# Performance work log

Hardware: AMD Instinct MI355X
Metric: run time of the kernel (lower is better)

The kernel has to match this reference:

```python
import jax, jax.numpy as jnp
import numpy as np

DIM_INPUT = 1024
DIM_LATENT = 1024
DIM_HEAD = 64
INNER = max(DIM_INPUT, DIM_LATENT)  # 1024
HEADS = INNER // DIM_HEAD           # 16
SCALE = DIM_HEAD ** -0.5
RMS_EPS = 1e-8
LN_EPS = 1e-5


def layernorm(x, w, b):
    mu = jnp.mean(x, axis=-1, keepdims=True)
    var = jnp.var(x, axis=-1, keepdims=True)
    return (x - mu) * jax.lax.rsqrt(var + LN_EPS) * w + b


def rmsnorm(x, gamma):
    # x / clamp(||x||_2 * d^-0.5, eps) * gamma  (per-head, last dim = DIM_HEAD)
    norm = jnp.linalg.norm(x, axis=-1, keepdims=True) * (DIM_HEAD ** -0.5)
    return x / jnp.maximum(norm, RMS_EPS) * gamma


def setup_inputs() -> dict:
    key = jax.random.key(0)
    ks = jax.random.split(key, 10)
    b, n, m = 4, 2048, 256
    x = jax.random.normal(ks[0], (b, n, DIM_INPUT), dtype=jnp.float32)
    latents_c1 = jax.random.normal(ks[1], (b, m, DIM_LATENT), dtype=jnp.float32)
    latents_c0 = jax.random.normal(ks[2], (b, m, DIM_LATENT), dtype=jnp.float32)
    consciousness_mask = jax.random.randint(ks[3], (b, n), 0, 2).astype(bool)
    s = 0.02
    Wq = jax.random.normal(ks[4], (DIM_LATENT, INNER), dtype=jnp.float32) * s
    Wkv = jax.random.normal(ks[5], (DIM_INPUT, 2 * INNER), dtype=jnp.float32) * s
    Wout = jax.random.normal(ks[6], (INNER, DIM_LATENT), dtype=jnp.float32) * s
    bout = jnp.zeros((DIM_LATENT,), dtype=jnp.float32)
    ln_x_w = jnp.ones((DIM_INPUT,), dtype=jnp.float32)
    ln_x_b = jnp.zeros((DIM_INPUT,), dtype=jnp.float32)
    ln_l_w = jnp.ones((DIM_LATENT,), dtype=jnp.float32)
    ln_l_b = jnp.zeros((DIM_LATENT,), dtype=jnp.float32)
    gamma_q = jnp.ones((DIM_HEAD,), dtype=jnp.float32)
    gamma_k = jnp.ones((DIM_HEAD,), dtype=jnp.float32)
    return dict(x=x, latents_c1=latents_c1, latents_c0=latents_c0,
                consciousness_mask=consciousness_mask,
                ln_x_w=ln_x_w, ln_x_b=ln_x_b, ln_l_w=ln_l_w, ln_l_b=ln_l_b,
                gamma_q=gamma_q, gamma_k=gamma_k,
                Wq=Wq, Wkv=Wkv, Wout=Wout, bout=bout)


def reference(x, latents_c1, latents_c0, consciousness_mask,
              ln_x_w, ln_x_b, ln_l_w, ln_l_b, gamma_q, gamma_k,
              Wq, Wkv, Wout, bout):
    b, n, _ = x.shape
    m = latents_c1.shape[1]
    x = layernorm(x, ln_x_w, ln_x_b)
    l1 = layernorm(latents_c1, ln_l_w, ln_l_b)
    l0 = layernorm(latents_c0, ln_l_w, ln_l_b)

    # projections -> heads
    q1 = (l1 @ Wq).reshape(b, m, HEADS, DIM_HEAD).transpose(0, 2, 1, 3)  # b h m d
    q0 = (l0 @ Wq).reshape(b, m, HEADS, DIM_HEAD).transpose(0, 2, 1, 3)
    kv = x @ Wkv                                                         # b n 2*inner
    k, v = jnp.split(kv, 2, axis=-1)
    k = k.reshape(b, n, HEADS, DIM_HEAD).transpose(0, 2, 1, 3)           # b h n d
    v = v.reshape(b, n, HEADS, DIM_HEAD).transpose(0, 2, 1, 3)

    qn1 = rmsnorm(q1, gamma_q) * SCALE
    qn0 = rmsnorm(q0, gamma_q) * SCALE
    kn = rmsnorm(k, gamma_k)

    attn1 = jnp.einsum('bhid,bhjd->bhij', qn1, kn)
    attn0 = jnp.einsum('bhid,bhjd->bhij', qn0, kn)

    neg = -jnp.finfo(attn1.dtype).max
    attn1 = jnp.where(consciousness_mask[:, None, None, :], attn1, neg)
    # NOTE: source only masks the c1 stream; c0 is left unmasked (faithful).

    attn1 = jax.nn.softmax(attn1, axis=-1)
    attn0 = jax.nn.softmax(attn0, axis=-1)

    o1 = jnp.einsum('bhij,bhjd->bhid', attn1, v).transpose(0, 2, 1, 3).reshape(b, m, INNER)
    o0 = jnp.einsum('bhij,bhjd->bhid', attn0, v).transpose(0, 2, 1, 3).reshape(b, m, INNER)
    return (o1 @ Wout + bout, o0 @ Wout + bout)
```

## Files before the change

kernel.cpp:

```cpp
#include <hip/hip_runtime.h>
#include <hip/hip_bf16.h>
#include <float.h>
#include <math.h>

#define BB 4
#define NN 2048
#define MM 256
#define DIN 1024
#define INNER 1024
#define NHEADS 16
#define DHEAD 64

typedef __attribute__((ext_vector_type(8))) short bf16x8;
typedef __attribute__((ext_vector_type(4))) float f32x4;
typedef __attribute__((ext_vector_type(4))) unsigned int u32x4;

__device__ __forceinline__ unsigned short f2bf(float f) {
    unsigned int u = __builtin_bit_cast(unsigned int, f);
    u = (u + 0x7fffu + ((u >> 16) & 1u)) >> 16;
    return (unsigned short)u;
}

__device__ __forceinline__ float fexp2(float x) {
#if __has_builtin(__builtin_amdgcn_exp2f)
    return __builtin_amdgcn_exp2f(x);
#else
    float r; asm("v_exp_f32 %0, %1" : "=v"(r) : "v"(x)); return r;
#endif
}

__device__ __forceinline__ unsigned int cvt_pk_bf16(float a, float b) {
    unsigned int r;
    asm("v_cvt_pk_bf16_f32 %0, %1, %2" : "=v"(r) : "v"(a), "v"(b));
    return r;
}

__device__ __forceinline__ void gload_lds16(const void* g, void* l) {
    __builtin_amdgcn_global_load_lds((__attribute__((address_space(1))) void*)(g),
                                     (__attribute__((address_space(3))) void*)(l),
                                     16, 0, 0);
}

#define LOG2E 1.4426950408889634f

__device__ __forceinline__ void ln_row(const float* __restrict__ srow,
                                       unsigned short* __restrict__ drow,
                                       const float* __restrict__ w,
                                       const float* __restrict__ bv) {
    const int tid = threadIdx.x;
    const float4 v = ((const float4*)srow)[tid];
    float sum = v.x + v.y + v.z + v.w;
    float sq  = v.x * v.x + v.y * v.y + v.z * v.z + v.w * v.w;
    #pragma unroll
    for (int off = 32; off; off >>= 1) {
        sum += __shfl_down(sum, off);
        sq  += __shfl_down(sq, off);
    }
    __shared__ float ls[4], lq[4];
    const int wv = tid >> 6;
    if ((tid & 63) == 0) { ls[wv] = sum; lq[wv] = sq; }
    __syncthreads();
    sum = ls[0] + ls[1] + ls[2] + ls[3];
    sq  = lq[0] + lq[1] + lq[2] + lq[3];
    const float mu  = sum * (1.0f / 1024.0f);
    const float var = sq * (1.0f / 1024.0f) - mu * mu;
    const float rs  = rsqrtf(var + 1e-5f);
    const float4 w4 = ((const float4*)w)[tid];
    const float4 b4 = ((const float4*)bv)[tid];
    ushort4 o;
    o.x = f2bf((v.x - mu) * rs * w4.x + b4.x);
    o.y = f2bf((v.y - mu) * rs * w4.y + b4.y);
    o.z = f2bf((v.z - mu) * rs * w4.z + b4.z);
    o.w = f2bf((v.w - mu) * rs * w4.w + b4.w);
    ((ushort4*)drow)[tid] = o;
}

__global__ __launch_bounds__(256) void ln_bf16_kernel(const float* __restrict__ src,
                                                      unsigned short* __restrict__ dst,
                                                      const float* __restrict__ w,
                                                      const float* __restrict__ bv) {
    const int row = blockIdx.x;
    ln_row(src + (size_t)row * 1024, dst + (size_t)row * 1024, w, bv);
}

__global__ __launch_bounds__(256) void ln2_bf16_kernel(const float* __restrict__ src1,
                                                       const float* __restrict__ src2,
                                                       int split,
                                                       unsigned short* __restrict__ dst,
                                                       const float* __restrict__ w,
                                                       const float* __restrict__ bv) {
    const int row = blockIdx.x;
    const float* s = (row < split) ? (src1 + (size_t)row * 1024)
                                   : (src2 + (size_t)(row - split) * 1024);
    ln_row(s, dst + (size_t)row * 1024, w, bv);
}

__global__ __launch_bounds__(256) void transpose_cast_kernel(const float* __restrict__ W,
                                                             unsigned short* __restrict__ WT,
                                                             int K, int N) {
    __shared__ float t[32][33];
    const int k0 = blockIdx.y * 32, n0 = blockIdx.x * 32;
    const int tx = threadIdx.x & 31, ty8 = threadIdx.x >> 5;
    #pragma unroll
    for (int i = 0; i < 4; i++) {
        const int k = ty8 + i * 8;
        t[k][tx] = W[(size_t)(k0 + k) * N + n0 + tx];
    }
    __syncthreads();
    #pragma unroll
    for (int i = 0; i < 4; i++) {
        const int n = ty8 + i * 8;
        WT[(size_t)(n0 + n) * K + k0 + tx] = f2bf(t[tx][n]);
    }
}

__global__ __launch_bounds__(256) void v_transpose_bf16(const unsigned short* __restrict__ vbh,
                                                        unsigned short* __restrict__ vth) {
    __shared__ unsigned short t[32][34];
    const int n0 = blockIdx.x * 32;
    const int d0 = blockIdx.y * 32;
    const int bh = blockIdx.z;
    const int b = bh >> 4, h = bh & 15;
    const int tx = threadIdx.x & 31, ty8 = threadIdx.x >> 5;
    #pragma unroll
    for (int i = 0; i < 4; i++) {
        const int nr = ty8 + i * 8;
        t[nr][tx] = vbh[(size_t)(b * NN + n0 + nr) * 1024 + h * 64 + d0 + tx];
    }
    __syncthreads();
    #pragma unroll
    for (int i = 0; i < 4; i++) {
        const int dr = ty8 + i * 8;
        vth[((size_t)(b * 16 + h) * 64 + d0 + dr) * 2048 + n0 + tx] = t[tx][dr];
    }
}

#define GEMM_STAGE(AS, BS, kt)                                                        \
    {                                                                                 \
        _Pragma("unroll")                                                             \
        for (int e = 0; e < 2; e++) {                                                 \
            const int r0 = (w * 2 + e) * 16;                                          \
            gload_lds16(Ag + (size_t)(r0 + srow) * K + (kt) + selt, &AS[r0 * 32]);    \
            gload_lds16(Bg + (size_t)(r0 + srow) * K + (kt) + selt, &BS[r0 * 32]);    \
        }                                                                             \
    }

#define GEMM_COMPUTE(AS, BS)                                                          \
    {                                                                                 \
        bf16x8 af[4], bfv[4];                                                         \
        _Pragma("unroll")                                                             \
        for (int m = 0; m < 4; m++)                                                   \
            af[m] = *(const bf16x8*)&AS[(wr * 64 + m * 16 + (l & 15)) * 32 + (l >> 4) * 8]; \
        _Pragma("unroll")                                                             \
        for (int n = 0; n < 4; n++)                                                   \
            bfv[n] = *(const bf16x8*)&BS[(wc * 64 + n * 16 + (l & 15)) * 32 + (l >> 4) * 8]; \
        _Pragma("unroll")                                                             \
        for (int m = 0; m < 4; m++)                                                   \
            _Pragma("unroll")                                                         \
            for (int n = 0; n < 4; n++)                                               \
                acc[m][n] = __builtin_amdgcn_mfma_f32_16x16x32_bf16(af[m], bfv[n], acc[m][n], 0, 0, 0); \
    }

template<int MODE>
__global__ __launch_bounds__(256) void gemm_bf16_kernel(const unsigned short* __restrict__ A,
                                                        const unsigned short* __restrict__ BT,
                                                        float* __restrict__ C,
                                                        unsigned short* __restrict__ outK,
                                                        unsigned short* __restrict__ outV,
                                                        int M, int N, int K,
                                                        const float* __restrict__ aux) {
    __shared__ __align__(16) unsigned short As0[128 * 32];
    __shared__ __align__(16) unsigned short As1[128 * 32];
    __shared__ __align__(16) unsigned short Bs0[128 * 32];
    __shared__ __align__(16) unsigned short Bs1[128 * 32];
    const int tid = threadIdx.x;
    const int l = tid & 63, w = tid >> 6;
    const int wr = w >> 1, wc = w & 1;

    const int gx = gridDim.x;
    const int flat = blockIdx.y * gx + blockIdx.x;
    const int cpx = (gx * gridDim.y) >> 3;
    const int swz = (flat & 7) * cpx + (flat >> 3);
    const int rb = (swz / gx) * 128, cb = (swz % gx) * 128;

    f32x4 acc[4][4];
    #pragma unroll
    for (int m = 0; m < 4; m++)
        #pragma unroll
        for (int n = 0; n < 4; n++) acc[m][n] = (f32x4){0.0f, 0.0f, 0.0f, 0.0f};

    const int srow = l >> 2;
    const int selt = (l & 3) * 8;
    const unsigned short* Ag = A + (size_t)rb * K;
    const unsigned short* Bg = BT + (size_t)cb * K;

    GEMM_STAGE(As0, Bs0, 0);
    __syncthreads();
    int kt = 0;
    for (; kt + 64 < K; kt += 64) {
        GEMM_STAGE(As1, Bs1, kt + 32);
        GEMM_COMPUTE(As0, Bs0);
        __syncthreads();
        GEMM_STAGE(As0, Bs0, kt + 64);
        GEMM_COMPUTE(As1, Bs1);
        __syncthreads();
    }
    GEMM_STAGE(As1, Bs1, kt + 32);
    GEMM_COMPUTE(As0, Bs0);
    __syncthreads();
    GEMM_COMPUTE(As1, Bs1);

    const int lx = l & 15;
    const int col0 = cb + wc * 64;
    const int row0 = rb + wr * 64 + (l >> 4) * 4;

    if constexpr (MODE == 0) {
        #pragma unroll
        for (int m = 0; m < 4; m++) {
            #pragma unroll
            for (int n = 0; n < 4; n++) {
                const int col = col0 + n * 16 + lx;
                const float badd = aux[col];
                #pragma unroll
                for (int r = 0; r < 4; r++)
                    C[(size_t)(row0 + m * 16 + r) * N + col] = acc[m][n][r] + badd;
            }
        }
    } else {
        const bool isK = (MODE == 2) || (col0 < (N >> 1));
        if (isK) {
            float g4[4];
            #pragma unroll
            for (int n = 0; n < 4; n++) g4[n] = aux[n * 16 + lx];
            const float fin = (MODE == 2) ? (0.125f * LOG2E) : 1.0f;
            #pragma unroll
            for (int m = 0; m < 4; m++) {
                #pragma unroll
                for (int r = 0; r < 4; r++) {
                    float ss = 0.0f;
                    #pragma unroll
                    for (int n = 0; n < 4; n++) ss += acc[m][n][r] * acc[m][n][r];
                    ss += __shfl_xor(ss, 1);
                    ss += __shfl_xor(ss, 2);
                    ss += __shfl_xor(ss, 4);
                    ss += __shfl_xor(ss, 8);
                    const float inv = fin / fmaxf(sqrtf(ss) * 0.125f, 1e-8f);
                    const size_t rbase = (size_t)(row0 + m * 16 + r) * 1024 + col0;
                    #pragma unroll
                    for (int n = 0; n < 4; n++)
                        outK[rbase + n * 16 + lx] = f2bf(acc[m][n][r] * inv * g4[n]);
                }
            }
        } else {
            const int colv = col0 - 1024;
            #pragma unroll
            for (int m = 0; m < 4; m++) {
                #pragma unroll
                for (int r = 0; r < 4; r++) {
                    const size_t rbase = (size_t)(row0 + m * 16 + r) * 1024 + colv;
                    #pragma unroll
                    for (int n = 0; n < 4; n++)
                        outV[rbase + n * 16 + lx] = f2bf(acc[m][n][r]);
                }
            }
        }
    }
}

__global__ __launch_bounds__(256) void attn_mfma_kernel(const unsigned short* __restrict__ qbh,
                                                        const unsigned short* __restrict__ kbh,
                                                        const unsigned short* __restrict__ vth,
                                                        const int* __restrict__ mask,
                                                        unsigned short* __restrict__ obuf) {
    const int bh = blockIdx.x;
    const int qt = blockIdx.y;
    const int sid = blockIdx.z;
    const int b = bh >> 4, h = bh & 15;
    const int tid = threadIdx.x;
    const int l = tid & 63, w = tid >> 6;
    const int lq = l & 15, g = l >> 4;

    __shared__ unsigned short Ks[64 * 64];
    __shared__ unsigned short Vts[64 * 64];
    __shared__ int Ms[64];

    bf16x8 aq[2];
    const size_t qrow = (size_t)((sid * BB + b) * MM + qt * 64 + w * 16 + lq);
    #pragma unroll
    for (int ks = 0; ks < 2; ks++)
        aq[ks] = *(const bf16x8*)&qbh[qrow * 1024 + h * 64 + ks * 32 + g * 8];

    f32x4 oacc[4];
    #pragma unroll
    for (int n = 0; n < 4; n++) oacc[n] = (f32x4){0.0f, 0.0f, 0.0f, 0.0f};
    float mrun = -FLT_MAX, lrun = 0.0f;

    for (int t0 = 0; t0 < NN; t0 += 64) {
        #pragma unroll
        for (int e = 0; e < 2; e++) {
            const int L = tid + 256 * e;
            const int row = L >> 3, c8 = L & 7;
            const bf16x8 kv8 = *(const bf16x8*)&kbh[(size_t)(b * NN + t0 + row) * 1024 + h * 64 + c8 * 8];
            *(bf16x8*)&Ks[row * 64 + ((c8 ^ (row & 7)) * 8)] = kv8;
            const bf16x8 vv8 = *(const bf16x8*)&vth[((size_t)(b * 16 + h) * 64 + row) * 2048 + t0 + c8 * 8];
            *(bf16x8*)&Vts[row * 64 + ((c8 ^ (row & 7)) * 8)] = vv8;
        }
        if (tid < 64) Ms[tid] = mask[b * NN + t0 + tid];
        __syncthreads();

        f32x4 st[4];
        #pragma unroll
        for (int j = 0; j < 4; j++) st[j] = (f32x4){0.0f, 0.0f, 0.0f, 0.0f};
        #pragma unroll
        for (int j = 0; j < 4; j++) {
            #pragma unroll
            for (int ks = 0; ks < 2; ks++) {
                const int row = j * 16 + lq;
                const bf16x8 kf = *(const bf16x8*)&Ks[row * 64 + (((ks * 4 + g) ^ (row & 7)) * 8)];
                st[j] = __builtin_amdgcn_mfma_f32_16x16x32_bf16(kf, aq[ks], st[j], 0, 0, 0);
            }
        }

        float p[4][4];
        if (sid == 0) {
            #pragma unroll
            for (int j = 0; j < 4; j++)
                #pragma unroll
                for (int r = 0; r < 4; r++)
                    p[j][r] = (Ms[j * 16 + g * 4 + r] == 0) ? -3.0e38f : st[j][r];
        } else {
            #pragma unroll
            for (int j = 0; j < 4; j++)
                #pragma unroll
                for (int r = 0; r < 4; r++) p[j][r] = st[j][r];
        }

        float mloc = fmaxf(fmaxf(p[0][0], p[0][1]), fmaxf(p[0][2], p[0][3]));
        #pragma unroll
        for (int j = 1; j < 4; j++)
            mloc = fmaxf(mloc, fmaxf(fmaxf(p[j][0], p[j][1]), fmaxf(p[j][2], p[j][3])));
        mloc = fmaxf(mloc, __shfl_xor(mloc, 16));
        mloc = fmaxf(mloc, __shfl_xor(mloc, 32));

        if (__any(mloc > mrun + 8.0f)) {
            const float mn = fmaxf(mrun, mloc);
            const float scal = fexp2(mrun - mn);
            mrun = mn;
            lrun *= scal;
            float oscal[4];
            #pragma unroll
            for (int r = 0; r < 4; r++) oscal[r] = __shfl(scal, g * 4 + r);
            #pragma unroll
            for (int n = 0; n < 4; n++)
                #pragma unroll
                for (int r = 0; r < 4; r++) oacc[n][r] *= oscal[r];
        }

        float rsum = 0.0f;
        #pragma unroll
        for (int j = 0; j < 4; j++)
            #pragma unroll
            for (int r = 0; r < 4; r++) { p[j][r] = fexp2(p[j][r] - mrun); rsum += p[j][r]; }
        rsum += __shfl_xor(rsum, 16);
        rsum += __shfl_xor(rsum, 32);
        lrun += rsum;

        unsigned int packed[4][2];
        #pragma unroll
        for (int jt = 0; jt < 4; jt++)
            #pragma unroll
            for (int hh = 0; hh < 2; hh++)
                packed[jt][hh] = cvt_pk_bf16(p[jt][2 * hh], p[jt][2 * hh + 1]);

        #pragma unroll
        for (int ks = 0; ks < 2; ks++) {
            unsigned int wds[4];
            #pragma unroll
            for (int wd = 0; wd < 4; wd++) {
                const int src = lq + 16 * ((g & 1) * 2 + (wd >> 1));
                const unsigned int vA = (unsigned int)__shfl((int)packed[ks * 2][wd & 1], src);
                const unsigned int vB = (unsigned int)__shfl((int)packed[ks * 2 + 1][wd & 1], src);
                wds[wd] = (g & 2) ? vB : vA;
            }
            const u32x4 tmp = {wds[0], wds[1], wds[2], wds[3]};
            const bf16x8 afP = __builtin_bit_cast(bf16x8, tmp);
            #pragma unroll
            for (int n = 0; n < 4; n++) {
                const int drow = n * 16 + lq;
                const bf16x8 bv = *(const bf16x8*)&Vts[drow * 64 + (((ks * 4 + g) ^ (drow & 7)) * 8)];
                oacc[n] = __builtin_amdgcn_mfma_f32_16x16x32_bf16(afP, bv, oacc[n], 0, 0, 0);
            }
        }
        __syncthreads();
    }

    const float il = 1.0f / lrun;
    float linv[4];
    #pragma unroll
    for (int r = 0; r < 4; r++) linv[r] = __shfl(il, g * 4 + r);
    unsigned short* ob = obuf + ((size_t)((sid * BB + b) * MM + qt * 64 + w * 16)) * 1024 + h * 64;
    #pragma unroll
    for (int n = 0; n < 4; n++)
        #pragma unroll
        for (int r = 0; r < 4; r++)
            ob[(size_t)(g * 4 + r) * 1024 + n * 16 + lq] = f2bf(oacc[n][r] * linv[r]);
}

extern "C" void kernel_launch(void* const* d_in, const int* in_sizes, int n_in,
                              void* d_out, int out_size, void* d_ws, size_t ws_size,
                              hipStream_t stream) {
    const float* x      = (const float*)d_in[0];
    const float* lc1    = (const float*)d_in[1];
    const float* lc0    = (const float*)d_in[2];
    const int*   mask   = (const int*)d_in[3];
    const float* ln_x_w = (const float*)d_in[4];
    const float* ln_x_b = (const float*)d_in[5];
    const float* ln_l_w = (const float*)d_in[6];
    const float* ln_l_b = (const float*)d_in[7];
    const float* g_q    = (const float*)d_in[8];
    const float* g_k    = (const float*)d_in[9];
    const float* Wq     = (const float*)d_in[10];
    const float* Wkv    = (const float*)d_in[11];
    const float* Wout   = (const float*)d_in[12];
    const float* bout   = (const float*)d_in[13];
    float* out = (float*)d_out;

    char* p = (char*)d_ws;
    unsigned short* xnb   = (unsigned short*)p; p += (size_t)8388608 * 2;
    unsigned short* latb  = (unsigned short*)p; p += (size_t)2097152 * 2;
    unsigned short* obb   = (unsigned short*)p; p += (size_t)2097152 * 2;
    unsigned short* WkvT  = (unsigned short*)p; p += (size_t)2097152 * 2;
    unsigned short* WqT   = (unsigned short*)p; p += (size_t)1048576 * 2;
    unsigned short* WoutT = (unsigned short*)p; p += (size_t)1048576 * 2;
    unsigned short* qbh   = (unsigned short*)p; p += (size_t)2097152 * 2;
    unsigned short* kbh   = (unsigned short*)p; p += (size_t)8388608 * 2;
    unsigned short* vbh   = (unsigned short*)p; p += (size_t)8388608 * 2;
    unsigned short* vth   = (unsigned short*)p; p += (size_t)8388608 * 2;

    ln_bf16_kernel<<<BB * NN, 256, 0, stream>>>(x, xnb, ln_x_w, ln_x_b);
    ln2_bf16_kernel<<<2 * BB * MM, 256, 0, stream>>>(lc1, lc0, BB * MM, latb, ln_l_w, ln_l_b);

    transpose_cast_kernel<<<dim3(2048 / 32, 1024 / 32), 256, 0, stream>>>(Wkv, WkvT, 1024, 2048);
    transpose_cast_kernel<<<dim3(1024 / 32, 1024 / 32), 256, 0, stream>>>(Wq, WqT, 1024, 1024);
    transpose_cast_kernel<<<dim3(1024 / 32, 1024 / 32), 256, 0, stream>>>(Wout, WoutT, 1024, 1024);

    gemm_bf16_kernel<1><<<dim3(2048 / 128, 8192 / 128), 256, 0, stream>>>(
        xnb, WkvT, nullptr, kbh, vbh, 8192, 2048, 1024, g_k);
    gemm_bf16_kernel<2><<<dim3(1024 / 128, 2048 / 128), 256, 0, stream>>>(
        latb, WqT, nullptr, qbh, nullptr, 2048, 1024, 1024, g_q);

    v_transpose_bf16<<<dim3(NN / 32, 2, BB * NHEADS), 256, 0, stream>>>(vbh, vth);

    attn_mfma_kernel<<<dim3(BB * NHEADS, MM / 64, 2), 256, 0, stream>>>(qbh, kbh, vth, mask, obb);

    gemm_bf16_kernel<0><<<dim3(1024 / 128, 2048 / 128), 256, 0, stream>>>(
        obb, WoutT, out, nullptr, nullptr, 2048, 1024, 1024, bout);
}
```

Before: 280.6 us.

## Double-buffer K/V tiles in attention and use smaller GEMM row tiles

The attention kernel now prefetches the next K, V and mask tile into registers while computing on the current LDS buffer. It writes them to a second LDS buffer, so each iteration needs one barrier instead of two. The Q-projection and output GEMMs become templated on BM and use 64-row tiles, doubling block count for these small (2048-row) GEMMs to fill more CUs. The trade-offs are more LDS and register use in attention and lower per-block reuse in the smaller GEMM tiles.

```diff
diff --git a/kernel.cpp b/kernel.cpp
--- a/kernel.cpp
+++ b/kernel.cpp
@@ -138,30 +138,34 @@
 #define GEMM_STAGE(AS, BS, kt)                                                        \
     {                                                                                 \
         _Pragma("unroll")                                                             \
+        for (int e = 0; e < EA; e++) {                                                \
+            const int r0 = (w * EA + e) * 16;                                         \
+            gload_lds16(Ag + (size_t)(r0 + srow) * K + (kt) + selt, &AS[r0 * 32]);    \
+        }                                                                             \
+        _Pragma("unroll")                                                             \
         for (int e = 0; e < 2; e++) {                                                 \
             const int r0 = (w * 2 + e) * 16;                                          \
-            gload_lds16(Ag + (size_t)(r0 + srow) * K + (kt) + selt, &AS[r0 * 32]);    \
             gload_lds16(Bg + (size_t)(r0 + srow) * K + (kt) + selt, &BS[r0 * 32]);    \
         }                                                                             \
     }
 
 #define GEMM_COMPUTE(AS, BS)                                                          \
     {                                                                                 \
-        bf16x8 af[4], bfv[4];                                                         \
+        bf16x8 af[MREP], bfv[4];                                                      \
         _Pragma("unroll")                                                             \
-        for (int m = 0; m < 4; m++)                                                   \
-            af[m] = *(const bf16x8*)&AS[(wr * 64 + m * 16 + (l & 15)) * 32 + (l >> 4) * 8]; \
+        for (int m = 0; m < MREP; m++)                                                \
+            af[m] = *(const bf16x8*)&AS[(wr * (BM / 2) + m * 16 + (l & 15)) * 32 + (l >> 4) * 8]; \
         _Pragma("unroll")                                                             \
         for (int n = 0; n < 4; n++)                                                   \
             bfv[n] = *(const bf16x8*)&BS[(wc * 64 + n * 16 + (l & 15)) * 32 + (l >> 4) * 8]; \
         _Pragma("unroll")                                                             \
-        for (int m = 0; m < 4; m++)                                                   \
+        for (int m = 0; m < MREP; m++)                                                \
             _Pragma("unroll")                                                         \
             for (int n = 0; n < 4; n++)                                               \
                 acc[m][n] = __builtin_amdgcn_mfma_f32_16x16x32_bf16(af[m], bfv[n], acc[m][n], 0, 0, 0); \
     }
 
-template<int MODE>
+template<int MODE, int BM>
 __global__ __launch_bounds__(256) void gemm_bf16_kernel(const unsigned short* __restrict__ A,
                                                         const unsigned short* __restrict__ BT,
                                                         float* __restrict__ C,
@@ -169,8 +173,10 @@
                                                         unsigned short* __restrict__ outV,
                                                         int M, int N, int K,
                                                         const float* __restrict__ aux) {
-    __shared__ __align__(16) unsigned short As0[128 * 32];
-    __shared__ __align__(16) unsigned short As1[128 * 32];
+    constexpr int MREP = BM / 32;
+    constexpr int EA = BM / 64;
+    __shared__ __align__(16) unsigned short As0[BM * 32];
+    __shared__ __align__(16) unsigned short As1[BM * 32];
     __shared__ __align__(16) unsigned short Bs0[128 * 32];
     __shared__ __align__(16) unsigned short Bs1[128 * 32];
     const int tid = threadIdx.x;
@@ -181,11 +187,11 @@
     const int flat = blockIdx.y * gx + blockIdx.x;
     const int cpx = (gx * gridDim.y) >> 3;
     const int swz = (flat & 7) * cpx + (flat >> 3);
-    const int rb = (swz / gx) * 128, cb = (swz % gx) * 128;
-
-    f32x4 acc[4][4];
-    #pragma unroll
-    for (int m = 0; m < 4; m++)
+    const int rb = (swz / gx) * BM, cb = (swz % gx) * 128;
+
+    f32x4 acc[MREP][4];
+    #pragma unroll
+    for (int m = 0; m < MREP; m++)
         #pragma unroll
         for (int n = 0; n < 4; n++) acc[m][n] = (f32x4){0.0f, 0.0f, 0.0f, 0.0f};
 
@@ -212,11 +218,11 @@
 
     const int lx = l & 15;
     const int col0 = cb + wc * 64;
-    const int row0 = rb + wr * 64 + (l >> 4) * 4;
+    const int row0 = rb + wr * (BM / 2) + (l >> 4) * 4;
 
     if constexpr (MODE == 0) {
         #pragma unroll
-        for (int m = 0; m < 4; m++) {
+        for (int m = 0; m < MREP; m++) {
             #pragma unroll
             for (int n = 0; n < 4; n++) {
                 const int col = col0 + n * 16 + lx;
@@ -234,7 +240,7 @@
             for (int n = 0; n < 4; n++) g4[n] = aux[n * 16 + lx];
             const float fin = (MODE == 2) ? (0.125f * LOG2E) : 1.0f;
             #pragma unroll
-            for (int m = 0; m < 4; m++) {
+            for (int m = 0; m < MREP; m++) {
                 #pragma unroll
                 for (int r = 0; r < 4; r++) {
                     float ss = 0.0f;
@@ -254,7 +260,7 @@
         } else {
             const int colv = col0 - 1024;
             #pragma unroll
-            for (int m = 0; m < 4; m++) {
+            for (int m = 0; m < MREP; m++) {
                 #pragma unroll
                 for (int r = 0; r < 4; r++) {
                     const size_t rbase = (size_t)(row0 + m * 16 + r) * 1024 + colv;
@@ -280,9 +286,8 @@
     const int l = tid & 63, w = tid >> 6;
     const int lq = l & 15, g = l >> 4;
 
-    __shared__ unsigned short Ks[64 * 64];
-    __shared__ unsigned short Vts[64 * 64];
-    __shared__ int Ms[64];
+    __shared__ __align__(16) unsigned short KVs[2][8192];
+    __shared__ int Ms[2][64];
 
     bf16x8 aq[2];
     const size_t qrow = (size_t)((sid * BB + b) * MM + qt * 64 + w * 16 + lq);
@@ -290,23 +295,48 @@
     for (int ks = 0; ks < 2; ks++)
         aq[ks] = *(const bf16x8*)&qbh[qrow * 1024 + h * 64 + ks * 32 + g * 8];
 
+    const int srow0 = tid >> 3, srow1 = (tid >> 3) + 32, sc8 = tid & 7;
+    const unsigned short* kgb = kbh + (size_t)(b * NN) * 1024 + h * 64;
+    const unsigned short* vgb = vth + ((size_t)(b * 16 + h) * 64) * 2048;
+    bf16x8 kreg0, kreg1, vreg0, vreg1;
+    int mreg = 0;
+
+#define ATT_LOAD(t0)                                                                  \
+    {                                                                                 \
+        kreg0 = *(const bf16x8*)&kgb[(size_t)((t0) + srow0) * 1024 + sc8 * 8];        \
+        kreg1 = *(const bf16x8*)&kgb[(size_t)((t0) + srow1) * 1024 + sc8 * 8];        \
+        vreg0 = *(const bf16x8*)&vgb[(size_t)srow0 * 2048 + (t0) + sc8 * 8];          \
+        vreg1 = *(const bf16x8*)&vgb[(size_t)srow1 * 2048 + (t0) + sc8 * 8];          \
+        if (tid < 64) mreg = mask[b * NN + (t0) + tid];                               \
+    }
+
+#define ATT_WRITE(buf)                                                                \
+    {                                                                                 \
+        unsigned short* kd = &KVs[buf][0];                                            \
+        *(bf16x8*)&kd[srow0 * 64 + ((sc8 ^ (srow0 & 7)) * 8)] = kreg0;                \
+        *(bf16x8*)&kd[srow1 * 64 + ((sc8 ^ (srow1 & 7)) * 8)] = kreg1;                \
+        unsigned short* vd = &KVs[buf][4096];                                         \
+        *(bf16x8*)&vd[srow0 * 64 + ((sc8 ^ (srow0 & 7)) * 8)] = vreg0;                \
+        *(bf16x8*)&vd[srow1 * 64 + ((sc8 ^ (srow1 & 7)) * 8)] = vreg1;                \
+        if (tid < 64) Ms[buf][tid] = mreg;                                            \
+    }
+
     f32x4 oacc[4];
     #pragma unroll
     for (int n = 0; n < 4; n++) oacc[n] = (f32x4){0.0f, 0.0f, 0.0f, 0.0f};
     float mrun = -FLT_MAX, lrun = 0.0f;
 
+    ATT_LOAD(0);
+    ATT_WRITE(0);
+    __syncthreads();
+    int cur = 0;
+
     for (int t0 = 0; t0 < NN; t0 += 64) {
-        #pragma unroll
-        for (int e = 0; e < 2; e++) {
-            const int L = tid + 256 * e;
-            const int row = L >> 3, c8 = L & 7;
-            const bf16x8 kv8 = *(const bf16x8*)&kbh[(size_t)(b * NN + t0 + row) * 1024 + h * 64 + c8 * 8];
-            *(bf16x8*)&Ks[row * 64 + ((c8 ^ (row & 7)) * 8)] = kv8;
-            const bf16x8 vv8 = *(const bf16x8*)&vth[((size_t)(b * 16 + h) * 64 + row) * 2048 + t0 + c8 * 8];
-            *(bf16x8*)&Vts[row * 64 + ((c8 ^ (row & 7)) * 8)] = vv8;
-        }
-        if (tid < 64) Ms[tid] = mask[b * NN + t0 + tid];
-        __syncthreads();
+        const bool nxt = (t0 + 64 < NN);
+        if (nxt) ATT_LOAD(t0 + 64);
+
+        const unsigned short* kcur = &KVs[cur][0];
+        const unsigned short* vcur = &KVs[cur][4096];
 
         f32x4 st[4];
         #pragma unroll
@@ -316,23 +346,24 @@
             #pragma unroll
             for (int ks = 0; ks < 2; ks++) {
                 const int row = j * 16 + lq;
-                const bf16x8 kf = *(const bf16x8*)&Ks[row * 64 + (((ks * 4 + g) ^ (row & 7)) * 8)];
+                const bf16x8 kf = *(const bf16x8*)&kcur[row * 64 + (((ks * 4 + g) ^ (row & 7)) * 8)];
                 st[j] = __builtin_amdgcn_mfma_f32_16x16x32_bf16(kf, aq[ks], st[j], 0, 0, 0);
             }
         }
 
         float p[4][4];
-        if (sid == 0) {
-            #pragma unroll
-            for (int j = 0; j < 4; j++)
-                #pragma unroll
-                for (int r = 0; r < 4; r++)
-                    p[j][r] = (Ms[j * 16 + g * 4 + r] == 0) ? -3.0e38f : st[j][r];
-        } else {
-            #pragma unroll
-            for (int j = 0; j < 4; j++)
+        #pragma unroll
+        for (int j = 0; j < 4; j++) {
+            if (sid == 0) {
+                const int4 mj = *(const int4*)&Ms[cur][j * 16 + g * 4];
+                p[j][0] = mj.x ? st[j][0] : -3.0e38f;
+                p[j][1] = mj.y ? st[j][1] : -3.0e38f;
+                p[j][2] = mj.z ? st[j][2] : -3.0e38f;
+                p[j][3] = mj.w ? st[j][3] : -3.0e38f;
+            } else {
                 #pragma unroll
                 for (int r = 0; r < 4; r++) p[j][r] = st[j][r];
+            }
         }
 
         float mloc = fmaxf(fmaxf(p[0][0], p[0][1]), fmaxf(p[0][2], p[0][3]));
@@ -387,11 +418,16 @@
             #pragma unroll
             for (int n = 0; n < 4; n++) {
                 const int drow = n * 16 + lq;
-                const bf16x8 bv = *(const bf16x8*)&Vts[drow * 64 + (((ks * 4 + g) ^ (drow & 7)) * 8)];
+                const bf16x8 bv = *(const bf16x8*)&vcur[drow * 64 + (((ks * 4 + g) ^ (drow & 7)) * 8)];
                 oacc[n] = __builtin_amdgcn_mfma_f32_16x16x32_bf16(afP, bv, oacc[n], 0, 0, 0);
             }
         }
-        __syncthreads();
+
+        if (nxt) {
+            ATT_WRITE(cur ^ 1);
+            __syncthreads();
+        }
+        cur ^= 1;
     }
 
     const float il = 1.0f / lrun;
@@ -444,15 +480,15 @@
     transpose_cast_kernel<<<dim3(1024 / 32, 1024 / 32), 256, 0, stream>>>(Wq, WqT, 1024, 1024);
     transpose_cast_kernel<<<dim3(1024 / 32, 1024 / 32), 256, 0, stream>>>(Wout, WoutT, 1024, 1024);
 
-    gemm_bf16_kernel<1><<<dim3(2048 / 128, 8192 / 128), 256, 0, stream>>>(
+    gemm_bf16_kernel<1, 128><<<dim3(2048 / 128, 8192 / 128), 256, 0, stream>>>(
         xnb, WkvT, nullptr, kbh, vbh, 8192, 2048, 1024, g_k);
-    gemm_bf16_kernel<2><<<dim3(1024 / 128, 2048 / 128), 256, 0, stream>>>(
+    gemm_bf16_kernel<2, 64><<<dim3(1024 / 128, 2048 / 64), 256, 0, stream>>>(
         latb, WqT, nullptr, qbh, nullptr, 2048, 1024, 1024, g_q);
 
     v_transpose_bf16<<<dim3(NN / 32, 2, BB * NHEADS), 256, 0, stream>>>(vbh, vth);
 
     attn_mfma_kernel<<<dim3(BB * NHEADS, MM / 64, 2), 256, 0, stream>>>(qbh, kbh, vth, mask, obb);
 
-    gemm_bf16_kernel<0><<<dim3(1024 / 128, 2048 / 128), 256, 0, stream>>>(
+    gemm_bf16_kernel<0, 64><<<dim3(1024 / 128, 2048 / 64), 256, 0, stream>>>(
         obb, WoutT, out, nullptr, nullptr, 2048, 1024, 1024, bout);
 }
```

Result: faster. 256.5 us (-8.6%).
